# Kernel optimization log

Measured on AMD Instinct MI355X. Metric: run time of the kernel, lower is better.

The kernel has to match this reference:

```python
import jax, jax.numpy as jnp
import numpy as np

NEG_SLOPE = 0.05

def _leaky(v):
    return jnp.where(v >= 0, v, NEG_SLOPE * v)

def setup_inputs() -> dict:
    key = jax.random.key(0)
    ks = jax.random.split(key, 9)
    B, N, D = 8, 96, 16
    H0, H1, OUT = 50, 50, 64
    x = jax.random.normal(ks[0], (B, N, D), dtype=jnp.float32)
    # dense 0/1 adjacency (float, used directly in matmuls), avg degree ~ 0.15*N
    adj = (jax.random.uniform(ks[1], (B, N, N)) < 0.15).astype(jnp.float32)
    h1 = 3 * D + 3          # 51
    h2 = 2 * D + H0 + 1     # 83
    h3 = D + H1             # 66
    W1 = jax.random.normal(ks[2], (h1, H0), dtype=jnp.float32) / np.sqrt(h1)
    b1 = jax.random.normal(ks[3], (H0,), dtype=jnp.float32) * 0.01
    W2 = jax.random.normal(ks[4], (h2, H1), dtype=jnp.float32) / np.sqrt(h2)
    b2 = jax.random.normal(ks[5], (H1,), dtype=jnp.float32) * 0.01
    W3 = jax.random.normal(ks[6], (h3, OUT), dtype=jnp.float32) / np.sqrt(h3)
    b3 = jax.random.normal(ks[7], (OUT,), dtype=jnp.float32) * 0.01
    return {"x": x, "adj": adj, "W1": W1, "b1": b1, "W2": W2, "b2": b2, "W3": W3, "b3": b3}

def reference(x, adj, W1, b1, W2, b2, W3, b3):
    # Faithful math of SpatialGraphConv.forward, with the O(N^4)/O(N^3)
    # broadcast+concat+GEMM algebraically decomposed into O(N^2) einsums
    # (identical result: the concat-GEMM is a sum of per-block contributions).
    B, N, D = x.shape
    H0 = W1.shape[1]
    # pairwise distances dis[b,i,j]
    diff = x[:, :, None, :] - x[:, None, :, :]            # (B,N,N,D)
    dis = jnp.sqrt(jnp.sum(diff * diff, axis=-1) + 1e-10)  # (B,N,N)
    # split W1 rows per concat block [x_i | x_j | x_k | d_ij | d_jk | d_ik]
    Wxi, Wxj, Wxk = W1[:D], W1[D:2 * D], W1[2 * D:3 * D]
    w_ij, w_jk, w_ik = W1[3 * D], W1[3 * D + 1], W1[3 * D + 2]  # (H0,)
    A = x @ Wxi   # (B,N,H0), indexed by i
    Bm = x @ Wxj  # (B,N,H0), indexed by j
    C = x @ Wxk   # (B,N,H0), indexed by k
    # m3_sum[b,i,j,h] = adj[b,i,j] * sum_k adj[b,j,k] * m3pre[b,i,j,k,h]
    deg = jnp.sum(adj, axis=-1)                           # (B,N): sum_k adj[b,j,k]
    sumC = jnp.einsum('bjk,bkh->bjh', adj, C)             # (B,N,H0)
    sd_jk = jnp.sum(adj * dis, axis=-1)                   # (B,N): sum_k adj[j,k]*dis[j,k]
    sd_ik = jnp.einsum('bik,bjk->bij', dis, adj)          # (B,N,N): sum_k adj[j,k]*dis[i,k]
    S = (deg[:, None, :, None] * (A[:, :, None, :] + Bm[:, None, :, :] + b1
                                   + dis[..., None] * w_ij)
         + sumC[:, None, :, :]
         + sd_jk[:, None, :, None] * w_jk
         + sd_ik[..., None] * w_ik)                        # (B,N,N,H0)
    m3_sum = _leaky(adj[..., None] * S)                    # (B,N,N,H0)
    # stage 2: pairwise concat [x_i | x_j | dis | m3_sum] -> MLP -> adj-masked sum over j
    xi = jnp.broadcast_to(x[:, :, None, :], (B, N, N, D))
    xj = jnp.broadcast_to(x[:, None, :, :], (B, N, N, D))
    feat2 = jnp.concatenate([xi, xj, dis[..., None], m3_sum], axis=-1)  # (B,N,N,2D+1+H0)
    m2 = feat2 @ W2 + b2                                   # (B,N,N,H1)
    m2_sum = _leaky(jnp.einsum('bijh,bij->bih', m2, adj))  # (B,N,H1)
    # stage 3: node-wise MLP
    m1 = _leaky(jnp.concatenate([x, m2_sum], axis=-1) @ W3 + b3)  # (B,N,OUT)
    return m1
```

## Files before the change

kernel.cpp:

```cpp
#include <hip/hip_runtime.h>
#include <math.h>

#define BB   8
#define NN   96
#define DD   16
#define H0D  50
#define H1D  50
#define OUTD 64
#define XP   17

typedef unsigned long long u64;


__device__ __forceinline__ float wave_reduce_sum(float v) {
    #pragma unroll
    for (int off = 1; off < 64; off <<= 1)
        v += __shfl_xor(v, off, 64);
    return v;
}

__global__ __launch_bounds__(64) void kA(
    const float* __restrict__ x, const float* __restrict__ adj,
    const float* __restrict__ W1,
    float* __restrict__ disws, u64* __restrict__ maskws,
    float* __restrict__ degws, float* __restrict__ sdjkws,
    float* __restrict__ nxws, float* __restrict__ APws)
{
    const int b = blockIdx.x / NN, j = blockIdx.x % NN;
    const int lane = threadIdx.x;
    __shared__ float sx[NN * XP];
    __shared__ float snx[DD];

    const float4* x4 = (const float4*)(x + (size_t)b * NN * DD);
    #pragma unroll
    for (int t = lane; t < NN * DD / 4; t += 64) {
        float4 v = x4[t];
        int row = t >> 2, d = (t & 3) * 4;
        float* p = &sx[row * XP + d];
        p[0] = v.x; p[1] = v.y; p[2] = v.z; p[3] = v.w;
    }
    const float* arow = adj + ((size_t)b * NN + j) * NN;
    float a0 = arow[lane];
    float a1 = (lane < NN - 64) ? arow[64 + lane] : 0.f;
    u64 m0 = __ballot(a0 != 0.f);
    u64 m1 = __ballot(a1 != 0.f);
    __syncthreads();

    const float* xj = &sx[j * XP];
    float d0, d1 = 0.f;
    {
        float s = 1e-10f;
        const float* xk = &sx[lane * XP];
        #pragma unroll
        for (int d = 0; d < DD; ++d) { float t = xj[d] - xk[d]; s += t * t; }
        d0 = sqrtf(s);
    }
    if (lane < NN - 64) {
        float s = 1e-10f;
        const float* xk = &sx[(64 + lane) * XP];
        #pragma unroll
        for (int d = 0; d < DD; ++d) { float t = xj[d] - xk[d]; s += t * t; }
        d1 = sqrtf(s);
    }
    float* drow = disws + ((size_t)b * NN + j) * NN;
    drow[lane] = d0;
    if (lane < NN - 64) drow[64 + lane] = d1;

    float deg = (float)(__popcll(m0) + __popcll(m1));
    float part = (((m0 >> lane) & 1) ? d0 : 0.f)
               + ((lane < 32 && ((m1 >> lane) & 1)) ? d1 : 0.f);
    float sdjk = wave_reduce_sum(part);
    if (lane == 0) {
        degws[b * NN + j]  = deg;
        sdjkws[b * NN + j] = sdjk;
        maskws[(b * NN + j) * 2 + 0] = m0;
        maskws[(b * NN + j) * 2 + 1] = m1;
    }

    {
        int c = lane >> 4, d = lane & 15;
        unsigned sm;
        if (c == 0)      sm = (unsigned)(m0 & 0xFFFFFFu);
        else if (c == 1) sm = (unsigned)((m0 >> 24) & 0xFFFFFFu);
        else if (c == 2) sm = (unsigned)((m0 >> 48) & 0xFFFFu) | ((unsigned)(m1 & 0xFFu) << 16);
        else             sm = (unsigned)((m1 >> 8) & 0xFFFFFFu);
        float s = 0.f;
        int base = c * 24;
        while (sm) {
            int k = base + __ffs(sm) - 1;
            sm &= sm - 1;
            s += sx[k * XP + d];
        }
        s += __shfl_xor(s, 16, 64);
        s += __shfl_xor(s, 32, 64);
        if (lane < DD) {
            snx[lane] = s;
            nxws[(b * NN + j) * DD + lane] = s;
        }
    }
    __syncthreads();

    if (lane < H0D) {
        float a = 0.f, bm = 0.f, sc = 0.f;
        #pragma unroll
        for (int d = 0; d < DD; ++d) {
            float xv = xj[d];
            a  += xv * W1[d * H0D + lane];
            bm += xv * W1[(DD + d) * H0D + lane];
            sc += snx[d] * W1[(2 * DD + d) * H0D + lane];
        }
        float* ap = APws + ((size_t)b * NN + j) * 128;
        ap[lane]      = a;
        ap[64 + lane] = deg * bm + sc;
    }
}

__global__ __launch_bounds__(64) void kB(
    const float* __restrict__ x,
    const float* __restrict__ W1, const float* __restrict__ b1,
    const float* __restrict__ W2, const float* __restrict__ b2,
    const float* __restrict__ W3, const float* __restrict__ b3,
    const float* __restrict__ disws, const u64* __restrict__ maskws,
    const float* __restrict__ degws, const float* __restrict__ sdjkws,
    const float* __restrict__ nxws, const float* __restrict__ APws,
    float* __restrict__ out)
{
    const int b = blockIdx.x / NN, i = blockIdx.x % NN;
    const int lane = threadIdx.x;
    __shared__ u64 sm0[NN], sm1[NN];
    __shared__ float sdis[NN], sdeg[NN], ssdjk[NN], ssdik[NN];
    __shared__ float smsum[H0D], sm2[H1D], sxi[DD], snxi[DD];

    const ulonglong2* mp = (const ulonglong2*)(maskws + (size_t)b * NN * 2);
    #pragma unroll
    for (int t = lane; t < NN; t += 64) {
        ulonglong2 m = mp[t];
        sm0[t] = m.x; sm1[t] = m.y;
    }
    const float* drow = disws + ((size_t)b * NN + i) * NN;
    sdis[lane] = drow[lane];
    if (lane < 32) sdis[64 + lane] = drow[64 + lane];
    sdeg[lane] = degws[b * NN + lane];
    if (lane < 32) sdeg[64 + lane] = degws[b * NN + 64 + lane];
    ssdjk[lane] = sdjkws[b * NN + lane];
    if (lane < 32) ssdjk[64 + lane] = sdjkws[b * NN + 64 + lane];
    if (lane < DD) {
        sxi[lane]  = x[((size_t)b * NN + i) * DD + lane];
        snxi[lane] = nxws[(b * NN + i) * DD + lane];
    }
    __syncthreads();

    {
        u64 mm0 = sm0[lane], mm1 = sm1[lane];
        float s = 0.f;
        while (mm0) { int k = __ffsll(mm0) - 1;      mm0 &= mm0 - 1; s += sdis[k]; }
        while (mm1) { int k = 64 + __ffsll(mm1) - 1; mm1 &= mm1 - 1; s += sdis[k]; }
        ssdik[lane] = s;
        if (lane < 32) {
            int j = 64 + lane;
            u64 n0 = sm0[j], n1 = sm1[j];
            float t = 0.f;
            while (n0) { int k = __ffsll(n0) - 1;      n0 &= n0 - 1; t += sdis[k]; }
            while (n1) { int k = 64 + __ffsll(n1) - 1; n1 &= n1 - 1; t += sdis[k]; }
            ssdik[j] = t;
        }
    }
    __syncthreads();

    {
        const int h = (lane < H0D) ? lane : 0;
        float ab  = APws[((size_t)b * NN + i) * 128 + h] + b1[h];
        float wij = W1[(3 * DD + 0) * H0D + h];
        float wjk = W1[(3 * DD + 1) * H0D + h];
        float wik = W1[(3 * DD + 2) * H0D + h];
        float msum = 0.f;
        u64 mm = sm0[i]; int base = 0;
        for (int half = 0; half < 2; ++half) {
            while (mm) {
                int j = base + __ffsll(mm) - 1;
                mm &= mm - 1;
                float S = sdeg[j] * (ab + sdis[j] * wij)
                        + APws[((size_t)b * NN + j) * 128 + 64 + h]
                        + ssdjk[j] * wjk + ssdik[j] * wik;
                msum += (S >= 0.f) ? S : 0.05f * S;
            }
            mm = sm1[i]; base = 64;
        }
        if (lane < H0D) smsum[lane] = msum;
    }
    __syncthreads();

    const float degi = sdeg[i], sdjki = ssdjk[i];
    if (lane < H1D) {
        float s = degi * b2[lane];
        #pragma unroll
        for (int d = 0; d < DD; ++d)
            s += degi * sxi[d] * W2[d * H1D + lane]
               + snxi[d] * W2[(DD + d) * H1D + lane];
        s += sdjki * W2[(2 * DD) * H1D + lane];
        for (int c = 0; c < H0D; ++c)
            s += smsum[c] * W2[(2 * DD + 1 + c) * H1D + lane];
        sm2[lane] = (s >= 0.f) ? s : 0.05f * s;
    }
    __syncthreads();

    {
        float s = b3[lane];
        #pragma unroll
        for (int d = 0; d < DD; ++d) s += sxi[d] * W3[d * OUTD + lane];
        for (int h = 0; h < H1D; ++h) s += sm2[h] * W3[(DD + h) * OUTD + lane];
        s = (s >= 0.f) ? s : 0.05f * s;
        out[((size_t)b * NN + i) * OUTD + lane] = s;
    }
}

extern "C" void kernel_launch(void* const* d_in, const int* in_sizes, int n_in,
                              void* d_out, int out_size, void* d_ws, size_t ws_size,
                              hipStream_t stream) {
    const float* x   = (const float*)d_in[0];
    const float* adj = (const float*)d_in[1];
    const float* W1  = (const float*)d_in[2];
    const float* b1  = (const float*)d_in[3];
    const float* W2  = (const float*)d_in[4];
    const float* b2  = (const float*)d_in[5];
    const float* W3  = (const float*)d_in[6];
    const float* b3  = (const float*)d_in[7];
    float* out = (float*)d_out;

    u64*   maskws = (u64*)d_ws;
    float* fbase  = (float*)((char*)d_ws + BB * NN * 2 * sizeof(u64));
    float* disws  = fbase;
    float* degws  = disws + BB * NN * NN;
    float* sdjkws = degws + BB * NN;
    float* nxws   = sdjkws + BB * NN;
    float* APws   = nxws + BB * NN * DD;

    kA<<<BB * NN, 64, 0, stream>>>(x, adj, W1, disws, maskws, degws, sdjkws, nxws, APws);
    kB<<<BB * NN, 64, 0, stream>>>(x, W1, b1, W2, b2, W3, b3,
                                   disws, maskws, degws, sdjkws, nxws, APws, out);
}
```

Before: 84.84 us.

## Fuse both kernels into one, recomputing per-batch node stats per block

Result: slower. 98.56 us (+16.2%).

```diff
diff --git a/kernel.cpp b/kernel.cpp
--- a/kernel.cpp
+++ b/kernel.cpp
@@ -8,210 +8,176 @@
 #define H1D  50
 #define OUTD 64
 #define XP   17
+#define GPB  12
+#define SZ   (NN / GPB)
+#define NW   8
+#define NT   (NW * 64)
 
 typedef unsigned long long u64;
 
 
-__device__ __forceinline__ float wave_reduce_sum(float v) {
-    #pragma unroll
-    for (int off = 1; off < 64; off <<= 1)
-        v += __shfl_xor(v, off, 64);
-    return v;
-}
+__global__ __launch_bounds__(NT) void kfused(
+    const float* __restrict__ x, const float* __restrict__ adj,
+    const float* __restrict__ W1, const float* __restrict__ b1,
+    const float* __restrict__ W2, const float* __restrict__ b2,
+    const float* __restrict__ W3, const float* __restrict__ b3,
+    float* __restrict__ out)
+{
+    const int b   = blockIdx.x / GPB;
+    const int s0  = (blockIdx.x % GPB) * SZ;
+    const int tid = threadIdx.x;
+    const int w   = tid >> 6, lane = tid & 63;
 
-__global__ __launch_bounds__(64) void kA(
-    const float* __restrict__ x, const float* __restrict__ adj,
-    const float* __restrict__ W1,
-    float* __restrict__ disws, u64* __restrict__ maskws,
-    float* __restrict__ degws, float* __restrict__ sdjkws,
-    float* __restrict__ nxws, float* __restrict__ APws)
-{
-    const int b = blockIdx.x / NN, j = blockIdx.x % NN;
-    const int lane = threadIdx.x;
     __shared__ float sx[NN * XP];
-    __shared__ float snx[DD];
+    __shared__ float sdis[SZ][NN + 1];
+    __shared__ u64   sm0[NN], sm1[NN];
+    __shared__ float sdeg[NN], ssdjk[NN];
+    __shared__ float snx[NN][DD];
+    __shared__ float sP[NN][H0D + 2];
 
     const float4* x4 = (const float4*)(x + (size_t)b * NN * DD);
-    #pragma unroll
-    for (int t = lane; t < NN * DD / 4; t += 64) {
-        float4 v = x4[t];
-        int row = t >> 2, d = (t & 3) * 4;
+    if (tid < NN * DD / 4) {
+        float4 v = x4[tid];
+        int row = tid >> 2, d = (tid & 3) * 4;
         float* p = &sx[row * XP + d];
         p[0] = v.x; p[1] = v.y; p[2] = v.z; p[3] = v.w;
     }
-    const float* arow = adj + ((size_t)b * NN + j) * NN;
-    float a0 = arow[lane];
-    float a1 = (lane < NN - 64) ? arow[64 + lane] : 0.f;
-    u64 m0 = __ballot(a0 != 0.f);
-    u64 m1 = __ballot(a1 != 0.f);
     __syncthreads();
 
-    const float* xj = &sx[j * XP];
-    float d0, d1 = 0.f;
-    {
-        float s = 1e-10f;
-        const float* xk = &sx[lane * XP];
-        #pragma unroll
-        for (int d = 0; d < DD; ++d) { float t = xj[d] - xk[d]; s += t * t; }
-        d0 = sqrtf(s);
-    }
-    if (lane < NN - 64) {
-        float s = 1e-10f;
-        const float* xk = &sx[(64 + lane) * XP];
-        #pragma unroll
-        for (int d = 0; d < DD; ++d) { float t = xj[d] - xk[d]; s += t * t; }
-        d1 = sqrtf(s);
-    }
-    float* drow = disws + ((size_t)b * NN + j) * NN;
-    drow[lane] = d0;
-    if (lane < NN - 64) drow[64 + lane] = d1;
+    const int h = (lane < H0D) ? lane : 0;
 
-    float deg = (float)(__popcll(m0) + __popcll(m1));
-    float part = (((m0 >> lane) & 1) ? d0 : 0.f)
-               + ((lane < 32 && ((m1 >> lane) & 1)) ? d1 : 0.f);
-    float sdjk = wave_reduce_sum(part);
-    if (lane == 0) {
-        degws[b * NN + j]  = deg;
-        sdjkws[b * NN + j] = sdjk;
-        maskws[(b * NN + j) * 2 + 0] = m0;
-        maskws[(b * NN + j) * 2 + 1] = m1;
+    float wB[DD], wC[DD];
+    #pragma unroll
+    for (int d = 0; d < DD; ++d) {
+        wB[d] = W1[(DD + d) * H0D + h];
+        wC[d] = W1[(2 * DD + d) * H0D + h];
     }
 
-    {
+    for (int j = w; j < NN; j += NW) {
+        const float* arow = adj + ((size_t)b * NN + j) * NN;
+        float a0 = arow[lane];
+        float a1 = (lane < NN - 64) ? arow[64 + lane] : 0.f;
+        u64 m0 = __ballot(a0 != 0.f);
+        u64 m1 = __ballot(a1 != 0.f);
+        float deg = (float)(__popcll(m0) + __popcll(m1));
+
+        const float* xj = &sx[j * XP];
+        float d0, d1 = 0.f;
+        {
+            float s = 1e-10f;
+            const float* xk = &sx[lane * XP];
+            #pragma unroll
+            for (int d = 0; d < DD; ++d) { float t = xj[d] - xk[d]; s += t * t; }
+            d0 = sqrtf(s);
+        }
+        if (lane < NN - 64) {
+            float s = 1e-10f;
+            const float* xk = &sx[(64 + lane) * XP];
+            #pragma unroll
+            for (int d = 0; d < DD; ++d) { float t = xj[d] - xk[d]; s += t * t; }
+            d1 = sqrtf(s);
+        }
+        if (j >= s0 && j < s0 + SZ) {
+            sdis[j - s0][lane] = d0;
+            if (lane < NN - 64) sdis[j - s0][64 + lane] = d1;
+        }
+
+        float part = (((m0 >> lane) & 1) ? d0 : 0.f)
+                   + ((lane < 32 && ((m1 >> lane) & 1)) ? d1 : 0.f);
+        #pragma unroll
+        for (int off = 1; off < 64; off <<= 1) part += __shfl_xor(part, off, 64);
+        if (lane == 0) {
+            sm0[j] = m0; sm1[j] = m1; sdeg[j] = deg; ssdjk[j] = part;
+        }
+
         int c = lane >> 4, d = lane & 15;
         unsigned sm;
         if (c == 0)      sm = (unsigned)(m0 & 0xFFFFFFu);
         else if (c == 1) sm = (unsigned)((m0 >> 24) & 0xFFFFFFu);
         else if (c == 2) sm = (unsigned)((m0 >> 48) & 0xFFFFu) | ((unsigned)(m1 & 0xFFu) << 16);
         else             sm = (unsigned)((m1 >> 8) & 0xFFFFFFu);
-        float s = 0.f;
+        float nxv = 0.f;
         int base = c * 24;
         while (sm) {
             int k = base + __ffs(sm) - 1;
             sm &= sm - 1;
-            s += sx[k * XP + d];
+            nxv += sx[k * XP + d];
         }
-        s += __shfl_xor(s, 16, 64);
-        s += __shfl_xor(s, 32, 64);
-        if (lane < DD) {
-            snx[lane] = s;
-            nxws[(b * NN + j) * DD + lane] = s;
+        nxv += __shfl_xor(nxv, 16, 64);
+        nxv += __shfl_xor(nxv, 32, 64);
+        if (lane < DD) snx[j][lane] = nxv;
+
+        float p = 0.f, bm = 0.f;
+        #pragma unroll
+        for (int d2 = 0; d2 < DD; ++d2) {
+            bm += sx[j * XP + d2] * wB[d2];
+            p  += __shfl(nxv, d2, 64) * wC[d2];
         }
+        if (lane < H0D) sP[j][lane] = deg * bm + p;
     }
     __syncthreads();
 
-    if (lane < H0D) {
-        float a = 0.f, bm = 0.f, sc = 0.f;
-        #pragma unroll
-        for (int d = 0; d < DD; ++d) {
-            float xv = xj[d];
-            a  += xv * W1[d * H0D + lane];
-            bm += xv * W1[(DD + d) * H0D + lane];
-            sc += snx[d] * W1[(2 * DD + d) * H0D + lane];
-        }
-        float* ap = APws + ((size_t)b * NN + j) * 128;
-        ap[lane]      = a;
-        ap[64 + lane] = deg * bm + sc;
-    }
-}
+    const int i  = s0 + w;
+    const int il = w;
 
-__global__ __launch_bounds__(64) void kB(
-    const float* __restrict__ x,
-    const float* __restrict__ W1, const float* __restrict__ b1,
-    const float* __restrict__ W2, const float* __restrict__ b2,
-    const float* __restrict__ W3, const float* __restrict__ b3,
-    const float* __restrict__ disws, const u64* __restrict__ maskws,
-    const float* __restrict__ degws, const float* __restrict__ sdjkws,
-    const float* __restrict__ nxws, const float* __restrict__ APws,
-    float* __restrict__ out)
-{
-    const int b = blockIdx.x / NN, i = blockIdx.x % NN;
-    const int lane = threadIdx.x;
-    __shared__ u64 sm0[NN], sm1[NN];
-    __shared__ float sdis[NN], sdeg[NN], ssdjk[NN], ssdik[NN];
-    __shared__ float smsum[H0D], sm2[H1D], sxi[DD], snxi[DD];
-
-    const ulonglong2* mp = (const ulonglong2*)(maskws + (size_t)b * NN * 2);
-    #pragma unroll
-    for (int t = lane; t < NN; t += 64) {
-        ulonglong2 m = mp[t];
-        sm0[t] = m.x; sm1[t] = m.y;
-    }
-    const float* drow = disws + ((size_t)b * NN + i) * NN;
-    sdis[lane] = drow[lane];
-    if (lane < 32) sdis[64 + lane] = drow[64 + lane];
-    sdeg[lane] = degws[b * NN + lane];
-    if (lane < 32) sdeg[64 + lane] = degws[b * NN + 64 + lane];
-    ssdjk[lane] = sdjkws[b * NN + lane];
-    if (lane < 32) ssdjk[64 + lane] = sdjkws[b * NN + 64 + lane];
-    if (lane < DD) {
-        sxi[lane]  = x[((size_t)b * NN + i) * DD + lane];
-        snxi[lane] = nxws[(b * NN + i) * DD + lane];
-    }
-    __syncthreads();
-
+    float sdik0 = 0.f, sdik1 = 0.f;
     {
         u64 mm0 = sm0[lane], mm1 = sm1[lane];
-        float s = 0.f;
-        while (mm0) { int k = __ffsll(mm0) - 1;      mm0 &= mm0 - 1; s += sdis[k]; }
-        while (mm1) { int k = 64 + __ffsll(mm1) - 1; mm1 &= mm1 - 1; s += sdis[k]; }
-        ssdik[lane] = s;
-        if (lane < 32) {
-            int j = 64 + lane;
-            u64 n0 = sm0[j], n1 = sm1[j];
-            float t = 0.f;
-            while (n0) { int k = __ffsll(n0) - 1;      n0 &= n0 - 1; t += sdis[k]; }
-            while (n1) { int k = 64 + __ffsll(n1) - 1; n1 &= n1 - 1; t += sdis[k]; }
-            ssdik[j] = t;
-        }
+        while (mm0) { int k = __ffsll(mm0) - 1;      mm0 &= mm0 - 1; sdik0 += sdis[il][k]; }
+        while (mm1) { int k = 64 + __ffsll(mm1) - 1; mm1 &= mm1 - 1; sdik0 += sdis[il][k]; }
     }
-    __syncthreads();
+    if (lane < NN - 64) {
+        int j1 = 64 + lane;
+        u64 mm0 = sm0[j1], mm1 = sm1[j1];
+        while (mm0) { int k = __ffsll(mm0) - 1;      mm0 &= mm0 - 1; sdik1 += sdis[il][k]; }
+        while (mm1) { int k = 64 + __ffsll(mm1) - 1; mm1 &= mm1 - 1; sdik1 += sdis[il][k]; }
+    }
 
+    float wA[DD];
+    #pragma unroll
+    for (int d = 0; d < DD; ++d) wA[d] = W1[d * H0D + h];
+    const float wij = W1[(3 * DD + 0) * H0D + h];
+    const float wjk = W1[(3 * DD + 1) * H0D + h];
+    const float wik = W1[(3 * DD + 2) * H0D + h];
+
+    float ab = b1[h];
+    #pragma unroll
+    for (int d = 0; d < DD; ++d) ab += sx[i * XP + d] * wA[d];
+
+    float msum = 0.f;
     {
-        const int h = (lane < H0D) ? lane : 0;
-        float ab  = APws[((size_t)b * NN + i) * 128 + h] + b1[h];
-        float wij = W1[(3 * DD + 0) * H0D + h];
-        float wjk = W1[(3 * DD + 1) * H0D + h];
-        float wik = W1[(3 * DD + 2) * H0D + h];
-        float msum = 0.f;
         u64 mm = sm0[i]; int base = 0;
         for (int half = 0; half < 2; ++half) {
             while (mm) {
                 int j = base + __ffsll(mm) - 1;
                 mm &= mm - 1;
-                float S = sdeg[j] * (ab + sdis[j] * wij)
-                        + APws[((size_t)b * NN + j) * 128 + 64 + h]
-                        + ssdjk[j] * wjk + ssdik[j] * wik;
+                float sdikj = (j < 64) ? __shfl(sdik0, j, 64)
+                                       : __shfl(sdik1, j - 64, 64);
+                float S = sdeg[j] * (ab + sdis[il][j] * wij) + sP[j][h]
+                        + ssdjk[j] * wjk + sdikj * wik;
                 msum += (S >= 0.f) ? S : 0.05f * S;
             }
             mm = sm1[i]; base = 64;
         }
-        if (lane < H0D) smsum[lane] = msum;
     }
-    __syncthreads();
 
     const float degi = sdeg[i], sdjki = ssdjk[i];
-    if (lane < H1D) {
-        float s = degi * b2[lane];
-        #pragma unroll
-        for (int d = 0; d < DD; ++d)
-            s += degi * sxi[d] * W2[d * H1D + lane]
-               + snxi[d] * W2[(DD + d) * H1D + lane];
-        s += sdjki * W2[(2 * DD) * H1D + lane];
-        for (int c = 0; c < H0D; ++c)
-            s += smsum[c] * W2[(2 * DD + 1 + c) * H1D + lane];
-        sm2[lane] = (s >= 0.f) ? s : 0.05f * s;
-    }
-    __syncthreads();
+    float s2 = degi * b2[h];
+    #pragma unroll
+    for (int d = 0; d < DD; ++d)
+        s2 += degi * sx[i * XP + d] * W2[d * H1D + h]
+            + snx[i][d] * W2[(DD + d) * H1D + h];
+    s2 += sdjki * W2[(2 * DD) * H1D + h];
+    for (int c = 0; c < H0D; ++c)
+        s2 += __shfl(msum, c, 64) * W2[(2 * DD + 1 + c) * H1D + h];
+    float m2v = (s2 >= 0.f) ? s2 : 0.05f * s2;
 
-    {
-        float s = b3[lane];
-        #pragma unroll
-        for (int d = 0; d < DD; ++d) s += sxi[d] * W3[d * OUTD + lane];
-        for (int h = 0; h < H1D; ++h) s += sm2[h] * W3[(DD + h) * OUTD + lane];
-        s = (s >= 0.f) ? s : 0.05f * s;
-        out[((size_t)b * NN + i) * OUTD + lane] = s;
-    }
+    float s3 = b3[lane];
+    #pragma unroll
+    for (int d = 0; d < DD; ++d) s3 += sx[i * XP + d] * W3[d * OUTD + lane];
+    for (int c = 0; c < H1D; ++c) s3 += __shfl(m2v, c, 64) * W3[(DD + c) * OUTD + lane];
+    s3 = (s3 >= 0.f) ? s3 : 0.05f * s3;
+    out[((size_t)b * NN + i) * OUTD + lane] = s3;
 }
 
 extern "C" void kernel_launch(void* const* d_in, const int* in_sizes, int n_in,
@@ -226,16 +192,7 @@
     const float* W3  = (const float*)d_in[6];
     const float* b3  = (const float*)d_in[7];
     float* out = (float*)d_out;
+    (void)d_ws; (void)ws_size;
 
-    u64*   maskws = (u64*)d_ws;
-    float* fbase  = (float*)((char*)d_ws + BB * NN * 2 * sizeof(u64));
-    float* disws  = fbase;
-    float* degws  = disws + BB * NN * NN;
-    float* sdjkws = degws + BB * NN;
-    float* nxws   = sdjkws + BB * NN;
-    float* APws   = nxws + BB * NN * DD;
-
-    kA<<<BB * NN, 64, 0, stream>>>(x, adj, W1, disws, maskws, degws, sdjkws, nxws, APws);
-    kB<<<BB * NN, 64, 0, stream>>>(x, W1, b1, W2, b2, W3, b3,
-                                   disws, maskws, degws, sdjkws, nxws, APws, out);
+    kfused<<<BB * GPB, NT, 0, stream>>>(x, adj, W1, b1, W2, b2, W3, b3, out);
 }
```

## Split kB j-loop across four waves and replace sparse bit-loops with dense predicated loops

Applied to the files above, without the earlier changes.

New measurement: 79.37 us. 1.07x faster.

```diff
diff --git a/kernel.cpp b/kernel.cpp
--- a/kernel.cpp
+++ b/kernel.cpp
@@ -29,6 +29,7 @@
     const int b = blockIdx.x / NN, j = blockIdx.x % NN;
     const int lane = threadIdx.x;
     __shared__ float sx[NN * XP];
+    __shared__ float sar[NN];
     __shared__ float snx[DD];
 
     const float4* x4 = (const float4*)(x + (size_t)b * NN * DD);
@@ -44,6 +45,8 @@
     float a1 = (lane < NN - 64) ? arow[64 + lane] : 0.f;
     u64 m0 = __ballot(a0 != 0.f);
     u64 m1 = __ballot(a1 != 0.f);
+    sar[lane] = a0;
+    if (lane < NN - 64) sar[64 + lane] = a1;
     __syncthreads();
 
     const float* xj = &sx[j * XP];
@@ -78,19 +81,11 @@
     }
 
     {
-        int c = lane >> 4, d = lane & 15;
-        unsigned sm;
-        if (c == 0)      sm = (unsigned)(m0 & 0xFFFFFFu);
-        else if (c == 1) sm = (unsigned)((m0 >> 24) & 0xFFFFFFu);
-        else if (c == 2) sm = (unsigned)((m0 >> 48) & 0xFFFFu) | ((unsigned)(m1 & 0xFFu) << 16);
-        else             sm = (unsigned)((m1 >> 8) & 0xFFFFFFu);
+        int c = lane >> 4, d = lane & 15, base = c * 24;
         float s = 0.f;
-        int base = c * 24;
-        while (sm) {
-            int k = base + __ffs(sm) - 1;
-            sm &= sm - 1;
-            s += sx[k * XP + d];
-        }
+        #pragma unroll
+        for (int t = 0; t < 24; ++t)
+            s += sar[base + t] * sx[(base + t) * XP + d];
         s += __shfl_xor(s, 16, 64);
         s += __shfl_xor(s, 32, 64);
         if (lane < DD) {
@@ -115,7 +110,7 @@
     }
 }
 
-__global__ __launch_bounds__(64) void kB(
+__global__ __launch_bounds__(256) void kB(
     const float* __restrict__ x,
     const float* __restrict__ W1, const float* __restrict__ b1,
     const float* __restrict__ W2, const float* __restrict__ b2,
@@ -126,72 +121,75 @@
     float* __restrict__ out)
 {
     const int b = blockIdx.x / NN, i = blockIdx.x % NN;
-    const int lane = threadIdx.x;
+    const int tid = threadIdx.x;
+    const int w = tid >> 6, lane = tid & 63;
     __shared__ u64 sm0[NN], sm1[NN];
     __shared__ float sdis[NN], sdeg[NN], ssdjk[NN], ssdik[NN];
-    __shared__ float smsum[H0D], sm2[H1D], sxi[DD], snxi[DD];
+    __shared__ float sxi[DD], snxi[DD];
+    __shared__ float smsum[4][H0D], smsumR[H0D], sm2[H1D];
 
     const ulonglong2* mp = (const ulonglong2*)(maskws + (size_t)b * NN * 2);
-    #pragma unroll
-    for (int t = lane; t < NN; t += 64) {
-        ulonglong2 m = mp[t];
-        sm0[t] = m.x; sm1[t] = m.y;
-    }
     const float* drow = disws + ((size_t)b * NN + i) * NN;
-    sdis[lane] = drow[lane];
-    if (lane < 32) sdis[64 + lane] = drow[64 + lane];
-    sdeg[lane] = degws[b * NN + lane];
-    if (lane < 32) sdeg[64 + lane] = degws[b * NN + 64 + lane];
-    ssdjk[lane] = sdjkws[b * NN + lane];
-    if (lane < 32) ssdjk[64 + lane] = sdjkws[b * NN + 64 + lane];
-    if (lane < DD) {
-        sxi[lane]  = x[((size_t)b * NN + i) * DD + lane];
-        snxi[lane] = nxws[(b * NN + i) * DD + lane];
-    }
-    __syncthreads();
-
-    {
-        u64 mm0 = sm0[lane], mm1 = sm1[lane];
+    if (tid < NN) {
+        ulonglong2 m = mp[tid];
+        sm0[tid] = m.x; sm1[tid] = m.y;
+        sdeg[tid]  = degws[b * NN + tid];
+        ssdjk[tid] = sdjkws[b * NN + tid];
+    } else if (tid < 2 * NN) {
+        int t = tid - NN;
+        sdis[t] = drow[t];
+    } else if (tid >= 224 && tid < 224 + DD) {
+        sxi[tid - 224] = x[((size_t)b * NN + i) * DD + (tid - 224)];
+    } else if (tid >= 240) {
+        snxi[tid - 240] = nxws[(b * NN + i) * DD + (tid - 240)];
+    }
+    __syncthreads();
+
+    if (tid < NN) {
+        u64 mm0 = sm0[tid], mm1 = sm1[tid];
         float s = 0.f;
-        while (mm0) { int k = __ffsll(mm0) - 1;      mm0 &= mm0 - 1; s += sdis[k]; }
-        while (mm1) { int k = 64 + __ffsll(mm1) - 1; mm1 &= mm1 - 1; s += sdis[k]; }
-        ssdik[lane] = s;
-        if (lane < 32) {
-            int j = 64 + lane;
-            u64 n0 = sm0[j], n1 = sm1[j];
-            float t = 0.f;
-            while (n0) { int k = __ffsll(n0) - 1;      n0 &= n0 - 1; t += sdis[k]; }
-            while (n1) { int k = 64 + __ffsll(n1) - 1; n1 &= n1 - 1; t += sdis[k]; }
-            ssdik[j] = t;
-        }
+        #pragma unroll
+        for (int k = 0; k < 64; ++k) {
+            s += (mm0 & 1) ? sdis[k] : 0.f;
+            mm0 >>= 1;
+        }
+        #pragma unroll
+        for (int k = 0; k < 32; ++k) {
+            s += (mm1 & 1) ? sdis[64 + k] : 0.f;
+            mm1 >>= 1;
+        }
+        ssdik[tid] = s;
     }
     __syncthreads();
 
     {
         const int h = (lane < H0D) ? lane : 0;
-        float ab  = APws[((size_t)b * NN + i) * 128 + h] + b1[h];
-        float wij = W1[(3 * DD + 0) * H0D + h];
-        float wjk = W1[(3 * DD + 1) * H0D + h];
-        float wik = W1[(3 * DD + 2) * H0D + h];
-        float msum = 0.f;
-        u64 mm = sm0[i]; int base = 0;
-        for (int half = 0; half < 2; ++half) {
-            while (mm) {
-                int j = base + __ffsll(mm) - 1;
-                mm &= mm - 1;
-                float S = sdeg[j] * (ab + sdis[j] * wij)
-                        + APws[((size_t)b * NN + j) * 128 + 64 + h]
-                        + ssdjk[j] * wjk + ssdik[j] * wik;
-                msum += (S >= 0.f) ? S : 0.05f * S;
-            }
-            mm = sm1[i]; base = 64;
-        }
-        if (lane < H0D) smsum[lane] = msum;
-    }
+        float ab = APws[((size_t)b * NN + i) * 128 + h] + b1[h];
+        const float wij = W1[(3 * DD + 0) * H0D + h];
+        const float wjk = W1[(3 * DD + 1) * H0D + h];
+        const float wik = W1[(3 * DD + 2) * H0D + h];
+        const u64 mi0 = sm0[i], mi1 = sm1[i];
+        float ms = 0.f;
+        const int j0 = w * 24;
+        #pragma unroll
+        for (int t = 0; t < 24; ++t) {
+            const int j = j0 + t;
+            bool e = (j < 64) ? ((mi0 >> j) & 1) : ((mi1 >> (j - 64)) & 1);
+            float gP = APws[((size_t)b * NN + j) * 128 + 64 + h];
+            float S = sdeg[j] * (ab + sdis[j] * wij) + gP
+                    + ssdjk[j] * wjk + ssdik[j] * wik;
+            float l = (S >= 0.f) ? S : 0.05f * S;
+            ms += e ? l : 0.f;
+        }
+        if (lane < H0D) smsum[w][lane] = ms;
+    }
+    __syncthreads();
+    if (tid < H0D)
+        smsumR[tid] = smsum[0][tid] + smsum[1][tid] + smsum[2][tid] + smsum[3][tid];
     __syncthreads();
 
     const float degi = sdeg[i], sdjki = ssdjk[i];
-    if (lane < H1D) {
+    if (w == 0 && lane < H1D) {
         float s = degi * b2[lane];
         #pragma unroll
         for (int d = 0; d < DD; ++d)
@@ -199,16 +197,16 @@
                + snxi[d] * W2[(DD + d) * H1D + lane];
         s += sdjki * W2[(2 * DD) * H1D + lane];
         for (int c = 0; c < H0D; ++c)
-            s += smsum[c] * W2[(2 * DD + 1 + c) * H1D + lane];
+            s += smsumR[c] * W2[(2 * DD + 1 + c) * H1D + lane];
         sm2[lane] = (s >= 0.f) ? s : 0.05f * s;
     }
     __syncthreads();
 
-    {
+    if (w == 0) {
         float s = b3[lane];
         #pragma unroll
         for (int d = 0; d < DD; ++d) s += sxi[d] * W3[d * OUTD + lane];
-        for (int h = 0; h < H1D; ++h) s += sm2[h] * W3[(DD + h) * OUTD + lane];
+        for (int c = 0; c < H1D; ++c) s += sm2[c] * W3[(DD + c) * OUTD + lane];
         s = (s >= 0.f) ? s : 0.05f * s;
         out[((size_t)b * NN + i) * OUTD + lane] = s;
     }
@@ -236,6 +234,6 @@
     float* APws   = nxws + BB * NN * DD;
 
     kA<<<BB * NN, 64, 0, stream>>>(x, adj, W1, disws, maskws, degws, sdjkws, nxws, APws);
-    kB<<<BB * NN, 64, 0, stream>>>(x, W1, b1, W2, b2, W3, b3,
-                                   disws, maskws, degws, sdjkws, nxws, APws, out);
-}
+    kB<<<BB * NN, 256, 0, stream>>>(x, W1, b1, W2, b2, W3, b3,
+                                    disws, maskws, degws, sdjkws, nxws, APws, out);
+}
```
